# Performance work log

Measured on AMD Instinct MI355X. Metric: run time of the kernel, lower is better.

## Reference

```python
import jax, jax.numpy as jnp
import numpy as np

POOL = 7  # fixed 7x7 output grid, hard-coded in the original layer


def _bin_bounds(step, rlen):
    # Replicates the original bin-corner logic + empty-bin adjustment.
    i = jnp.arange(POOL, dtype=jnp.int32)
    s = i * step
    e = jnp.where(i < POOL - 1, (i + 1) * step, rlen)
    empty = s == e
    # original: grow end by 1 if room, else shrink start by 1
    e = jnp.where(empty & (e < rlen), e + 1, e)
    s = jnp.where(empty & ~(e > (i * step)) , s, s)  # no-op placeholder for clarity
    s = jnp.where(empty & ((i * step) == e), (i * step) - 1, jnp.where(empty, i * step, s))
    # simpler equivalent: if still empty after trying to grow end, shrink start
    s0 = i * step
    e0 = jnp.where(i < POOL - 1, (i + 1) * step, rlen)
    grow = empty & (e0 < rlen)
    e = jnp.where(grow, e0 + 1, e0)
    s = jnp.where(empty & ~grow, s0 - 1, s0)
    return s, e


def _pool_one(roi, fm):
    # fm: [H, W, C]; roi: [4] normalized (y1, x1, y2, x2)
    H, W, C = fm.shape
    h0 = (H * roi[0]).astype(jnp.int32)  # tf.cast to int32 truncates (floor for >=0)
    w0 = (W * roi[1]).astype(jnp.int32)
    h1 = (H * roi[2]).astype(jnp.int32)
    w1 = (W * roi[3]).astype(jnp.int32)
    rh = h1 - h0
    rw = w1 - w0
    hstep = rh // POOL
    wstep = rw // POOL
    sh, eh = _bin_bounds(hstep, rh)  # [7], region-relative
    sw, ew = _bin_bounds(wstep, rw)
    hidx = jnp.arange(H, dtype=jnp.int32)
    widx = jnp.arange(W, dtype=jnp.int32)
    rmask = (hidx[None, :] >= (h0 + sh)[:, None]) & (hidx[None, :] < (h0 + eh)[:, None])  # [7,H]
    cmask = (widx[None, :] >= (w0 + sw)[:, None]) & (widx[None, :] < (w0 + ew)[:, None])  # [7,W]
    neg = jnp.asarray(-jnp.inf, fm.dtype)
    # max over rows for each of the 7 row-bins: [7, W, C]
    t = jnp.max(jnp.where(rmask[:, :, None, None], fm[None, :, :, :], neg), axis=1)
    # max over cols for each of the 7 col-bins: [7, 7, C]
    out = jnp.max(jnp.where(cmask[None, :, :, None], t[:, None, :, :], neg), axis=2)
    return out


def setup_inputs() -> dict:
    key = jax.random.key(0)
    k_f, k_y, k_x, k_h, k_w = jax.random.split(key, 5)
    H, W, C, N = 50, 50, 1024, 300
    features = jax.random.normal(k_f, (1, H, W, C), dtype=jnp.float32)
    # well-formed normalized ROIs: y1 < y2, x1 < x2, extent in [0.2, 0.55]
    y1 = jax.random.uniform(k_y, (N,), minval=0.0, maxval=0.45)
    x1 = jax.random.uniform(k_x, (N,), minval=0.0, maxval=0.45)
    hh = jax.random.uniform(k_h, (N,), minval=0.2, maxval=0.55)
    ww = jax.random.uniform(k_w, (N,), minval=0.2, maxval=0.55)
    rois = jnp.stack([y1, x1, jnp.minimum(y1 + hh, 1.0), jnp.minimum(x1 + ww, 1.0)], axis=1).astype(jnp.float32)
    return {"features": features, "rois": rois}


def reference(features, rois):
    fm = jnp.squeeze(features, axis=0)  # [H, W, C]
    # sequential over ROIs (mirrors tf.while_loop), fully vectorized per ROI
    pooled = jax.lax.map(lambda r: _pool_one(r, fm), rois)  # [N, 7, 7, C]
    return pooled
```

## Files before the change

kernel.cpp:

```cpp
#include <hip/hip_runtime.h>
#include <math.h>

#define POOL 7
#define FH 50
#define FW 50
#define FC 1024

__global__ __launch_bounds__(256) void roipool_kernel(
    const float* __restrict__ fm,
    const float* __restrict__ rois,
    float* __restrict__ out)
{
    const int bid = blockIdx.x;
    const int n  = bid / 49;
    const int ij = bid - n * 49;
    const int i  = ij / 7;
    const int j  = ij - i * 7;

    const float4 roi = reinterpret_cast<const float4*>(rois)[n];
    const int h0 = (int)((float)FH * roi.x);
    const int w0 = (int)((float)FW * roi.y);
    const int h1 = (int)((float)FH * roi.z);
    const int w1 = (int)((float)FW * roi.w);
    const int rh = h1 - h0;
    const int rw = w1 - w0;
    const int hstep = rh / POOL;
    const int wstep = rw / POOL;

    int sh = i * hstep;
    int eh = (i < POOL - 1) ? (i + 1) * hstep : rh;
    if (sh == eh) { if (eh < rh) eh += 1; else sh -= 1; }
    int sw = j * wstep;
    int ew = (j < POOL - 1) ? (j + 1) * wstep : rw;
    if (sw == ew) { if (ew < rw) ew += 1; else sw -= 1; }

    const int r0 = max(0, h0 + sh);
    const int r1 = min(FH, h0 + eh);
    const int c0 = max(0, w0 + sw);
    const int c1 = min(FW, w0 + ew);

    const int t = threadIdx.x;

    float4 acc;
    acc.x = -INFINITY; acc.y = -INFINITY; acc.z = -INFINITY; acc.w = -INFINITY;

    for (int r = r0; r < r1; ++r) {
        const float4* row = reinterpret_cast<const float4*>(fm + ((size_t)(r * FW)) * FC);
        for (int c = c0; c < c1; ++c) {
            float4 v = row[c * (FC / 4) + t];
            acc.x = fmaxf(acc.x, v.x);
            acc.y = fmaxf(acc.y, v.y);
            acc.z = fmaxf(acc.z, v.z);
            acc.w = fmaxf(acc.w, v.w);
        }
    }

    reinterpret_cast<float4*>(out + (size_t)bid * FC)[t] = acc;
}

extern "C" void kernel_launch(void* const* d_in, const int* in_sizes, int n_in,
                              void* d_out, int out_size, void* d_ws, size_t ws_size,
                              hipStream_t stream) {
    const float* features = (const float*)d_in[0];
    const float* rois     = (const float*)d_in[1];
    float* out            = (float*)d_out;
    const int N = in_sizes[1] / 4;

    dim3 grid(N * POOL * POOL);
    dim3 block(256);
    roipool_kernel<<<grid, block, 0, stream>>>(features, rois, out);
}
```

Measured before the change: 110.9 us.

## Use 64-thread blocks with 4 channel vectors per thread, unroll columns, nontemporal stores

Each block shrinks to a single 64-thread wavefront, and each thread now handles four float4 channel groups instead of one. The column loop is unrolled by two, so eight independent loads are in flight per iteration to raise memory-level parallelism. Output writes use nontemporal stores so they do not pollute the cache holding the feature map. The trade-off is fewer threads in flight per bin and more registers per thread.

```diff
diff --git a/kernel.cpp b/kernel.cpp
--- a/kernel.cpp
+++ b/kernel.cpp
@@ -5,8 +5,20 @@
 #define FH 50
 #define FW 50
 #define FC 1024
+#define FC4 (FC / 4)
 
-__global__ __launch_bounds__(256) void roipool_kernel(
+typedef float vf4 __attribute__((ext_vector_type(4)));
+
+static __device__ __forceinline__ vf4 vmax4(vf4 a, vf4 b) {
+    vf4 r;
+    r.x = fmaxf(a.x, b.x);
+    r.y = fmaxf(a.y, b.y);
+    r.z = fmaxf(a.z, b.z);
+    r.w = fmaxf(a.w, b.w);
+    return r;
+}
+
+__global__ __launch_bounds__(64) void roipool_kernel(
     const float* __restrict__ fm,
     const float* __restrict__ rois,
     float* __restrict__ out)
@@ -41,21 +53,48 @@
 
     const int t = threadIdx.x;
 
-    float4 acc;
-    acc.x = -INFINITY; acc.y = -INFINITY; acc.z = -INFINITY; acc.w = -INFINITY;
+    vf4 acc0 = {-INFINITY, -INFINITY, -INFINITY, -INFINITY};
+    vf4 acc1 = acc0, acc2 = acc0, acc3 = acc0;
+
+    const vf4* fm4 = reinterpret_cast<const vf4*>(fm);
 
     for (int r = r0; r < r1; ++r) {
-        const float4* row = reinterpret_cast<const float4*>(fm + ((size_t)(r * FW)) * FC);
-        for (int c = c0; c < c1; ++c) {
-            float4 v = row[c * (FC / 4) + t];
-            acc.x = fmaxf(acc.x, v.x);
-            acc.y = fmaxf(acc.y, v.y);
-            acc.z = fmaxf(acc.z, v.z);
-            acc.w = fmaxf(acc.w, v.w);
+        const vf4* rowp = fm4 + (size_t)(r * FW) * FC4;
+        int c = c0;
+        for (; c + 1 < c1; c += 2) {
+            const vf4* p0 = rowp + (size_t)c * FC4;
+            const vf4* p1 = rowp + (size_t)(c + 1) * FC4;
+            vf4 a0 = p0[t];
+            vf4 a1 = p0[t + 64];
+            vf4 a2 = p0[t + 128];
+            vf4 a3 = p0[t + 192];
+            vf4 b0 = p1[t];
+            vf4 b1 = p1[t + 64];
+            vf4 b2 = p1[t + 128];
+            vf4 b3 = p1[t + 192];
+            acc0 = vmax4(acc0, vmax4(a0, b0));
+            acc1 = vmax4(acc1, vmax4(a1, b1));
+            acc2 = vmax4(acc2, vmax4(a2, b2));
+            acc3 = vmax4(acc3, vmax4(a3, b3));
+        }
+        if (c < c1) {
+            const vf4* p0 = rowp + (size_t)c * FC4;
+            vf4 a0 = p0[t];
+            vf4 a1 = p0[t + 64];
+            vf4 a2 = p0[t + 128];
+            vf4 a3 = p0[t + 192];
+            acc0 = vmax4(acc0, a0);
+            acc1 = vmax4(acc1, a1);
+            acc2 = vmax4(acc2, a2);
+            acc3 = vmax4(acc3, a3);
         }
     }
 
-    reinterpret_cast<float4*>(out + (size_t)bid * FC)[t] = acc;
+    vf4* o = reinterpret_cast<vf4*>(out) + (size_t)bid * FC4;
+    __builtin_nontemporal_store(acc0, o + t);
+    __builtin_nontemporal_store(acc1, o + t + 64);
+    __builtin_nontemporal_store(acc2, o + t + 128);
+    __builtin_nontemporal_store(acc3, o + t + 192);
 }
 
 extern "C" void kernel_launch(void* const* d_in, const int* in_sizes, int n_in,
@@ -67,6 +106,6 @@
     const int N = in_sizes[1] / 4;
 
     dim3 grid(N * POOL * POOL);
-    dim3 block(256);
+    dim3 block(64);
     roipool_kernel<<<grid, block, 0, stream>>>(features, rois, out);
 }
```

New measurement: 102.5 us. 7.5% less time.

## Assign one wave per bin-chunk, unroll column loop, use nontemporal stores

Applied to the files above, without the earlier changes.

Changes the work decomposition so each 64-lane wave handles a 256-channel chunk of one output bin, with four bins per block and channel chunks split across grid.y. The inner column loop is unrolled by two to keep two independent loads in flight, and output writes use nontemporal stores to avoid polluting cache with write-once data. The aim is better load balance across variable-size bins and more memory-level parallelism, at the cost of waves in a block diverging in loop trip counts.

```diff
diff --git a/kernel.cpp b/kernel.cpp
--- a/kernel.cpp
+++ b/kernel.cpp
@@ -5,15 +5,35 @@
 #define FH 50
 #define FW 50
 #define FC 1024
+#define FC4 (FC / 4)
+#define CHUNKS 4
+#define F4C 64
+
+typedef float vf4 __attribute__((ext_vector_type(4)));
+
+static __device__ __forceinline__ vf4 vmax4(vf4 a, vf4 b) {
+    vf4 r;
+    r.x = fmaxf(a.x, b.x);
+    r.y = fmaxf(a.y, b.y);
+    r.z = fmaxf(a.z, b.z);
+    r.w = fmaxf(a.w, b.w);
+    return r;
+}
 
 __global__ __launch_bounds__(256) void roipool_kernel(
     const float* __restrict__ fm,
     const float* __restrict__ rois,
-    float* __restrict__ out)
+    float* __restrict__ out,
+    int nbins)
 {
-    const int bid = blockIdx.x;
-    const int n  = bid / 49;
-    const int ij = bid - n * 49;
+    const int wave = threadIdx.x >> 6;
+    const int lane = threadIdx.x & 63;
+    const int gid  = blockIdx.x * 4 + wave;
+    if (gid >= nbins) return;
+    const int chunk = blockIdx.y;
+
+    const int n  = gid / 49;
+    const int ij = gid - n * 49;
     const int i  = ij / 7;
     const int j  = ij - i * 7;
 
@@ -39,23 +59,27 @@
     const int c0 = max(0, w0 + sw);
     const int c1 = min(FW, w0 + ew);
 
-    const int t = threadIdx.x;
+    const int f4 = chunk * F4C + lane;
 
-    float4 acc;
-    acc.x = -INFINITY; acc.y = -INFINITY; acc.z = -INFINITY; acc.w = -INFINITY;
+    vf4 acc = {-INFINITY, -INFINITY, -INFINITY, -INFINITY};
+
+    const vf4* fm4 = reinterpret_cast<const vf4*>(fm);
 
     for (int r = r0; r < r1; ++r) {
-        const float4* row = reinterpret_cast<const float4*>(fm + ((size_t)(r * FW)) * FC);
-        for (int c = c0; c < c1; ++c) {
-            float4 v = row[c * (FC / 4) + t];
-            acc.x = fmaxf(acc.x, v.x);
-            acc.y = fmaxf(acc.y, v.y);
-            acc.z = fmaxf(acc.z, v.z);
-            acc.w = fmaxf(acc.w, v.w);
+        const vf4* rowp = fm4 + (size_t)(r * FW) * FC4 + f4;
+        int c = c0;
+        for (; c + 1 < c1; c += 2) {
+            vf4 a = rowp[(size_t)c * FC4];
+            vf4 b = rowp[(size_t)(c + 1) * FC4];
+            acc = vmax4(acc, vmax4(a, b));
+        }
+        if (c < c1) {
+            acc = vmax4(acc, rowp[(size_t)c * FC4]);
         }
     }
 
-    reinterpret_cast<float4*>(out + (size_t)bid * FC)[t] = acc;
+    vf4* o = reinterpret_cast<vf4*>(out) + (size_t)gid * FC4 + f4;
+    __builtin_nontemporal_store(acc, o);
 }
 
 extern "C" void kernel_launch(void* const* d_in, const int* in_sizes, int n_in,
@@ -66,7 +90,8 @@
     float* out            = (float*)d_out;
     const int N = in_sizes[1] / 4;
 
-    dim3 grid(N * POOL * POOL);
+    const int nbins = N * POOL * POOL;
+    dim3 grid((nbins + 3) / 4, CHUNKS);
     dim3 block(256);
-    roipool_kernel<<<grid, block, 0, stream>>>(features, rois, out);
+    roipool_kernel<<<grid, block, 0, stream>>>(features, rois, out, nbins);
 }
```

Result: faster. 100.8 us (-9.1%).
